# Kernel tuning notes

Hardware: AMD Instinct MI355X
Metric: run time of the kernel (lower is better)

Reference implementation:

```python
import jax, jax.numpy as jnp
import numpy as np

TTT_LR = 0.01
LN_EPS = 1e-5


def setup_inputs() -> dict:
    key = jax.random.key(0)
    ks = jax.random.split(key, 4)
    B, S, D, DS = 4, 2048, 1024, 64
    sc = 1.0 / np.sqrt(D).astype(np.float32)
    return {
        "x": jax.random.normal(ks[0], (B, S, D), dtype=jnp.float32),
        "Wk": jax.random.normal(ks[1], (DS, D), dtype=jnp.float32) * sc,
        "bk": jnp.zeros((DS,), jnp.float32),
        "Wv": jax.random.normal(ks[2], (D, D), dtype=jnp.float32) * sc,
        "bv": jnp.zeros((D,), jnp.float32),
        "Wq": jax.random.normal(ks[3], (DS, D), dtype=jnp.float32) * sc,
        "bq": jnp.zeros((DS,), jnp.float32),
        "gamma": jnp.ones((D,), jnp.float32),
        "beta": jnp.zeros((D,), jnp.float32),
    }


def reference(x, Wk, bk, Wv, bv, Wq, bq, gamma, beta):
    B, S, D = x.shape
    DS = Wk.shape[0]
    # LayerNorm over last dim
    mu = jnp.mean(x, axis=-1, keepdims=True)
    var = jnp.mean((x - mu) ** 2, axis=-1, keepdims=True)
    h = (x - mu) * jax.lax.rsqrt(var + LN_EPS) * gamma + beta
    # projections: keys/queries (B,S,DS), values (B,S,D)
    keys = jnp.einsum('bsd,ed->bse', h, Wk) + bk
    values = jnp.einsum('bsd,ed->bse', h, Wv) + bv
    queries = jnp.einsum('bsd,ed->bse', h, Wq) + bq

    def step(W, qkv):
        # W: (B, D, DS) fast-weight state
        q_t, k_t, v_t = qkv  # (B,DS), (B,DS), (B,D)
        y_t = jnp.einsum('bds,bs->bd', W, q_t)      # read with query
        pred = jnp.einsum('bds,bs->bd', W, k_t)     # predict with key
        err = pred - v_t                             # (B, D)
        W = W - TTT_LR * err[:, :, None] * k_t[:, None, :]  # rank-1 grad step
        return W, y_t

    W0 = jnp.zeros((B, D, DS), x.dtype)
    # scan over time: inputs as (S, B, ...)
    qs = jnp.swapaxes(queries, 0, 1)
    ks_ = jnp.swapaxes(keys, 0, 1)
    vs = jnp.swapaxes(values, 0, 1)
    _, ys = jax.lax.scan(step, W0, (qs, ks_, vs))   # ys: (S, B, D)
    y = jnp.swapaxes(ys, 0, 1)
    return x + y
```

## Files before the change

### kernel.cpp

```cpp
#include <hip/hip_runtime.h>
#include <hip/hip_bf16.h>

#define TTT_LR 0.01f
#define LN_EPS 1e-5f

#define BB 4
#define SS 2048
#define DD 1024
#define DSZ 64
#define CHUNK 64
#define NC (SS / CHUNK)
#define NCAT 1152
#define NCVT (NCAT * DD / 4 / 256)
#define MiB (1024ull * 1024ull)

typedef __hip_bfloat16 bf16;
typedef __bf16 bf16x8 __attribute__((ext_vector_type(8)));
typedef float f32x4 __attribute__((ext_vector_type(4)));

__device__ __forceinline__ void gload_lds16(const void* g, void* l) {
    __builtin_amdgcn_global_load_lds(
        (const __attribute__((address_space(1))) unsigned int*)g,
        (__attribute__((address_space(3))) unsigned int*)l, 16, 0, 0);
}

__global__ __launch_bounds__(256) void pre_kernel(
    const float* __restrict__ Wk, const float* __restrict__ Wq,
    const float* __restrict__ Wv, bf16* __restrict__ Wcat,
    const float* __restrict__ x, const float* __restrict__ gamma,
    const float* __restrict__ beta, bf16* __restrict__ hb)
{
    __shared__ float wsum[4], wsum2[4];
    const int tid = threadIdx.x;

    if (blockIdx.x < NCVT) {
        const int i = blockIdx.x * 256 + tid;
        const int idx = i * 4;
        const int row = idx >> 10, col = idx & 1023;
        const float* src = (row < 64)  ? (Wk + (size_t)row * DD)
                         : (row < 128) ? (Wq + (size_t)(row - 64) * DD)
                                       : (Wv + (size_t)(row - 128) * DD);
        float4 v = *reinterpret_cast<const float4*>(src + col);
        bf16 h4[4] = {__float2bfloat16(v.x), __float2bfloat16(v.y),
                      __float2bfloat16(v.z), __float2bfloat16(v.w)};
        *reinterpret_cast<ushort4*>(Wcat + idx) = *reinterpret_cast<ushort4*>(h4);
        return;
    }

    const int row = blockIdx.x - NCVT;
    const int lane = tid & 63, wave = tid >> 6;

    float4 v0 = *reinterpret_cast<const float4*>(x + (size_t)row * DD + tid * 4);
    float s = v0.x + v0.y + v0.z + v0.w;
    float s2 = fmaf(v0.x, v0.x, fmaf(v0.y, v0.y, fmaf(v0.z, v0.z, v0.w * v0.w)));
    #pragma unroll
    for (int off = 32; off > 0; off >>= 1) {
        s  += __shfl_down(s, off, 64);
        s2 += __shfl_down(s2, off, 64);
    }
    if (lane == 0) { wsum[wave] = s; wsum2[wave] = s2; }
    __syncthreads();
    s  = wsum[0] + wsum[1] + wsum[2] + wsum[3];
    s2 = wsum2[0] + wsum2[1] + wsum2[2] + wsum2[3];
    const float mu = s * (1.0f / DD);
    const float rs = rsqrtf(s2 * (1.0f / DD) - mu * mu + LN_EPS);

    float4 g  = *reinterpret_cast<const float4*>(gamma + tid * 4);
    float4 be = *reinterpret_cast<const float4*>(beta + tid * 4);
    bf16 h4[4];
    h4[0] = __float2bfloat16((v0.x - mu) * rs * g.x + be.x);
    h4[1] = __float2bfloat16((v0.y - mu) * rs * g.y + be.y);
    h4[2] = __float2bfloat16((v0.z - mu) * rs * g.z + be.z);
    h4[3] = __float2bfloat16((v0.w - mu) * rs * g.w + be.w);
    *reinterpret_cast<ushort4*>(hb + (size_t)row * DD + tid * 4) =
        *reinterpret_cast<ushort4*>(h4);
}

__global__ __launch_bounds__(256) void kqv_kernel(
    const bf16* __restrict__ h, const bf16* __restrict__ Wcat,
    const float* __restrict__ bk, const float* __restrict__ bq,
    const float* __restrict__ bv,
    float* __restrict__ kbuf, float* __restrict__ qbuf, bf16* __restrict__ vbuf16)
{
    __shared__ bf16 Ash[128 * 64];
    __shared__ bf16 Bsh[128 * 64];
    const int tid = threadIdx.x, lane = tid & 63, wave = tid >> 6;
    const int m = lane & 15, quad = lane >> 4;
    const int wr = wave >> 1, wc = wave & 1;
    const int m0 = blockIdx.y * 128;
    const int n0 = blockIdx.x * 128;

    const int srow = wave * 8 + (lane >> 3);
    const int scb = lane & 7;

    f32x4 acc[4][4] = {};

    for (int k0 = 0; k0 < DD; k0 += 64) {
        __syncthreads();
        #pragma unroll
        for (int i = 0; i < 4; ++i) {
            const int row = i * 32 + srow;
            const int g16 = scb ^ (row & 7);
            gload_lds16(h    + (size_t)(m0 + row) * DD + k0 + g16 * 8,
                        (char*)Ash + (size_t)(i * 32 + wave * 8) * 128);
            gload_lds16(Wcat + (size_t)(n0 + row) * DD + k0 + g16 * 8,
                        (char*)Bsh + (size_t)(i * 32 + wave * 8) * 128);
        }
        __syncthreads();
        #pragma unroll
        for (int ks = 0; ks < 2; ++ks) {
            bf16x8 af[4], bfr[4];
            #pragma unroll
            for (int mt = 0; mt < 4; ++mt) {
                const int row = wr * 64 + mt * 16 + m;
                const int kb = (ks * 4 + quad) ^ (row & 7);
                af[mt] = *reinterpret_cast<const bf16x8*>(&Ash[row * 64 + kb * 8]);
            }
            #pragma unroll
            for (int nt = 0; nt < 4; ++nt) {
                const int row = wc * 64 + nt * 16 + m;
                const int kb = (ks * 4 + quad) ^ (row & 7);
                bfr[nt] = *reinterpret_cast<const bf16x8*>(&Bsh[row * 64 + kb * 8]);
            }
            #pragma unroll
            for (int mt = 0; mt < 4; ++mt)
                #pragma unroll
                for (int nt = 0; nt < 4; ++nt)
                    acc[mt][nt] = __builtin_amdgcn_mfma_f32_16x16x32_bf16(
                        af[mt], bfr[nt], acc[mt][nt], 0, 0, 0);
        }
    }

    #pragma unroll
    for (int nt = 0; nt < 4; ++nt) {
        const int n = n0 + wc * 64 + nt * 16 + m;
        if (n < 64) {
            const float bias = bk[n];
            #pragma unroll
            for (int mt = 0; mt < 4; ++mt) {
                const int row = m0 + wr * 64 + mt * 16 + quad * 4;
                #pragma unroll
                for (int r = 0; r < 4; ++r)
                    kbuf[(size_t)(row + r) * DSZ + n] = acc[mt][nt][r] + bias;
            }
        } else if (n < 128) {
            const float bias = bq[n - 64];
            #pragma unroll
            for (int mt = 0; mt < 4; ++mt) {
                const int row = m0 + wr * 64 + mt * 16 + quad * 4;
                #pragma unroll
                for (int r = 0; r < 4; ++r)
                    qbuf[(size_t)(row + r) * DSZ + (n - 64)] = acc[mt][nt][r] + bias;
            }
        } else {
            const float bias = bv[n - 128];
            #pragma unroll
            for (int mt = 0; mt < 4; ++mt) {
                const int row = m0 + wr * 64 + mt * 16 + quad * 4;
                #pragma unroll
                for (int r = 0; r < 4; ++r)
                    vbuf16[(size_t)(row + r) * DD + (n - 128)] =
                        __float2bfloat16(acc[mt][nt][r] + bias);
            }
        }
    }
}

__global__ __launch_bounds__(256) void prep_kernel(
    const float* __restrict__ kbuf, const float* __restrict__ qbuf,
    bf16* __restrict__ Mb16, bf16* __restrict__ AMb16,
    bf16* __restrict__ Bb16, bf16* __restrict__ Qtb16, bf16* __restrict__ Ktb16)
{
    __shared__ bf16 K16[64 * 72];
    __shared__ bf16 Kt16[64 * 72];
    __shared__ bf16 Q16[64 * 72];
    __shared__ bf16 Astl[64 * 72];
    __shared__ bf16 Minv16[64 * 72];
    __shared__ bf16 MinvT16[64 * 72];
    __shared__ bf16 BnegT[64 * 72];
    __shared__ float Gf[64 * 65];
    __shared__ float Mf[64 * 65];

    const int c = blockIdx.x, b = blockIdx.y;
    const int tid = threadIdx.x, lane = tid & 63, w = tid >> 6;
    const int m = lane & 15, quad = lane >> 4;
    const float* kp = kbuf + ((size_t)b * SS + c * 64) * DSZ;
    const float* qp = qbuf + ((size_t)b * SS + c * 64) * DSZ;
    const size_t cb = ((size_t)b * NC + c) * 4096;

    #pragma unroll
    for (int it = 0; it < 4; ++it) {
        const int f4 = tid + it * 256;
        const int t = f4 >> 4;
        const int s = (f4 & 15) * 4;
        float4 kv = *reinterpret_cast<const float4*>(kp + t * DSZ + s);
        float4 qv = *reinterpret_cast<const float4*>(qp + t * DSZ + s);
        bf16 kb4[4] = {__float2bfloat16(kv.x), __float2bfloat16(kv.y),
                       __float2bfloat16(kv.z), __float2bfloat16(kv.w)};
        bf16 qb4[4] = {__float2bfloat16(qv.x), __float2bfloat16(qv.y),
                       __float2bfloat16(qv.z), __float2bfloat16(qv.w)};
        *reinterpret_cast<ushort4*>(&K16[t * 72 + s]) = *reinterpret_cast<ushort4*>(kb4);
        *reinterpret_cast<ushort4*>(&Q16[t * 72 + s]) = *reinterpret_cast<ushort4*>(qb4);
        #pragma unroll
        for (int i = 0; i < 4; ++i) Kt16[(s + i) * 72 + t] = kb4[i];
    }
    __syncthreads();

    bf16x8 afK[2], afQ[2], bfK[4][2];
    #pragma unroll
    for (int ks = 0; ks < 2; ++ks) {
        afK[ks] = *reinterpret_cast<const bf16x8*>(&K16[(w * 16 + m) * 72 + ks * 32 + quad * 8]);
        afQ[ks] = *reinterpret_cast<const bf16x8*>(&Q16[(w * 16 + m) * 72 + ks * 32 + quad * 8]);
        #pragma unroll
        for (int nt = 0; nt < 4; ++nt)
            bfK[nt][ks] = *reinterpret_cast<const bf16x8*>(&K16[(nt * 16 + m) * 72 + ks * 32 + quad * 8]);
    }
    f32x4 gacc[4] = {}, aacc[4] = {};
    #pragma unroll
    for (int ks = 0; ks < 2; ++ks)
        #pragma unroll
        for (int nt = 0; nt < 4; ++nt) {
            gacc[nt] = __builtin_amdgcn_mfma_f32_16x16x32_bf16(afK[ks], bfK[nt][ks], gacc[nt], 0, 0, 0);
            aacc[nt] = __builtin_amdgcn_mfma_f32_16x16x32_bf16(afQ[ks], bfK[nt][ks], aacc[nt], 0, 0, 0);
        }
    #pragma unroll
    for (int nt = 0; nt < 4; ++nt)
        #pragma unroll
        for (int r = 0; r < 4; ++r) {
            const int t = w * 16 + quad * 4 + r, j = nt * 16 + m;
            Gf[t * 65 + j] = TTT_LR * gacc[nt][r];
            Astl[t * 72 + j] = __float2bfloat16(j < t ? aacc[nt][r] : 0.f);
        }
    __syncthreads();

    if (tid < 64) {
        for (int t = 0; t < 64; ++t) {
            float acc = (t == tid) ? 1.f : 0.f;
            for (int i = 0; i < t; ++i)
                acc = fmaf(-Gf[t * 65 + i], Mf[i * 65 + tid], acc);
            Mf[t * 65 + tid] = acc;
        }
    }
    __syncthreads();

    #pragma unroll
    for (int it = 0; it < 16; ++it) {
        const int e = tid + it * 256;
        const int t = e >> 6, j = e & 63;
        const bf16 vb = __float2bfloat16(TTT_LR * Mf[t * 65 + j]);
        Minv16[t * 72 + j] = vb;
        MinvT16[j * 72 + t] = vb;
        Mb16[cb + e] = vb;
        const unsigned short ku =
            *reinterpret_cast<const unsigned short*>(&Kt16[t * 72 + j]) ^ 0x8000u;
        *reinterpret_cast<unsigned short*>(&Ktb16[cb + e]) = ku;
    }
    __syncthreads();

    bf16x8 afM[2], afA[2], bfKt[4][2], bfMt[4][2];
    #pragma unroll
    for (int ks = 0; ks < 2; ++ks) {
        afM[ks] = *reinterpret_cast<const bf16x8*>(&Minv16[(w * 16 + m) * 72 + ks * 32 + quad * 8]);
        afA[ks] = *reinterpret_cast<const bf16x8*>(&Astl[(w * 16 + m) * 72 + ks * 32 + quad * 8]);
        #pragma unroll
        for (int nt = 0; nt < 4; ++nt) {
            bfKt[nt][ks] = *reinterpret_cast<const bf16x8*>(&Kt16[(nt * 16 + m) * 72 + ks * 32 + quad * 8]);
            bfMt[nt][ks] = *reinterpret_cast<const bf16x8*>(&MinvT16[(nt * 16 + m) * 72 + ks * 32 + quad * 8]);
        }
    }
    f32x4 bacc[4] = {};
    #pragma unroll
    for (int ks = 0; ks < 2; ++ks)
        #pragma unroll
        for (int nt = 0; nt < 4; ++nt)
            bacc[nt] = __builtin_amdgcn_mfma_f32_16x16x32_bf16(afM[ks], bfKt[nt][ks], bacc[nt], 0, 0, 0);
    #pragma unroll
    for (int nt = 0; nt < 4; ++nt)
        #pragma unroll
        for (int r = 0; r < 4; ++r) {
            const int t = w * 16 + quad * 4 + r, s = nt * 16 + m;
            Bb16[cb + t * 64 + s] = __float2bfloat16(bacc[nt][r]);
            BnegT[s * 72 + t] = __float2bfloat16(-bacc[nt][r]);
        }
    __syncthreads();

    f32x4 qtacc[4], amacc[4] = {};
    #pragma unroll
    for (int nt = 0; nt < 4; ++nt)
        #pragma unroll
        for (int r = 0; r < 4; ++r)
            qtacc[nt][r] = qp[(w * 16 + quad * 4 + r) * DSZ + nt * 16 + m];
    #pragma unroll
    for (int ks = 0; ks < 2; ++ks)
        #pragma unroll
        for (int nt = 0; nt < 4; ++nt) {
            const bf16x8 bfBn = *reinterpret_cast<const bf16x8*>(
                &BnegT[(nt * 16 + m) * 72 + ks * 32 + quad * 8]);
            qtacc[nt] = __builtin_amdgcn_mfma_f32_16x16x32_bf16(afA[ks], bfBn, qtacc[nt], 0, 0, 0);
            amacc[nt] = __builtin_amdgcn_mfma_f32_16x16x32_bf16(afA[ks], bfMt[nt][ks], amacc[nt], 0, 0, 0);
        }
    #pragma unroll
    for (int nt = 0; nt < 4; ++nt)
        #pragma unroll
        for (int r = 0; r < 4; ++r) {
            const int t = w * 16 + quad * 4 + r, s = nt * 16 + m;
            Qtb16[cb + t * 64 + s] = __float2bfloat16(qtacc[nt][r]);
            AMb16[cb + t * 64 + s] = __float2bfloat16(amacc[nt][r]);
        }
}

struct ChunkRegs {
    bf16x8 M0, M1, A0, A1, B0, B1, Q0, Q1, K0, K1;
    alignas(8) unsigned short va[4], vb[4];
    float xld[4];
};

__global__ __launch_bounds__(256) void scan2_kernel(
    const bf16* __restrict__ Mb16, const bf16* __restrict__ AMb16,
    const bf16* __restrict__ Bb16, const bf16* __restrict__ Qtb16,
    const bf16* __restrict__ Ktb16, const bf16* __restrict__ v16,
    const float* __restrict__ x, float* __restrict__ out)
{
    __shared__ bf16 Zsh[16][72];
    __shared__ bf16 Psh[16][72];
    __shared__ bf16 Vsh[2][16][72];
    const int dblk = blockIdx.x, b = blockIdx.y;
    const int tid = threadIdx.x, lane = tid & 63, w = tid >> 6;
    const int m = lane & 15, quad = lane >> 4;
    const int d0 = dblk * 16;
    const int arow = w * 16 + m;
    const int trow = w * 16 + quad * 4;

    const bool vact = tid < 128;
    const int vj2 = (tid & 31) * 2;
    const int vd = (tid >> 5) * 4;

    f32x4 zacc = {0.f, 0.f, 0.f, 0.f};
    for (int i = tid; i < 16 * 72; i += 256)
        (&Zsh[0][0])[i] = __float2bfloat16(0.f);

    auto load_chunk = [&](int c, ChunkRegs& R) {
        const size_t cb = ((size_t)b * NC + c) * 4096;
        const size_t rowbase = (size_t)b * SS + (size_t)c * 64;
        R.M0 = *reinterpret_cast<const bf16x8*>(Mb16 + cb + arow * 64 + quad * 8);
        R.M1 = *reinterpret_cast<const bf16x8*>(Mb16 + cb + arow * 64 + 32 + quad * 8);
        R.A0 = *reinterpret_cast<const bf16x8*>(AMb16 + cb + arow * 64 + quad * 8);
        R.A1 = *reinterpret_cast<const bf16x8*>(AMb16 + cb + arow * 64 + 32 + quad * 8);
        R.B0 = *reinterpret_cast<const bf16x8*>(Bb16 + cb + arow * 64 + quad * 8);
        R.B1 = *reinterpret_cast<const bf16x8*>(Bb16 + cb + arow * 64 + 32 + quad * 8);
        R.Q0 = *reinterpret_cast<const bf16x8*>(Qtb16 + cb + arow * 64 + quad * 8);
        R.Q1 = *reinterpret_cast<const bf16x8*>(Qtb16 + cb + arow * 64 + 32 + quad * 8);
        R.K0 = *reinterpret_cast<const bf16x8*>(Ktb16 + cb + arow * 64 + quad * 8);
        R.K1 = *reinterpret_cast<const bf16x8*>(Ktb16 + cb + arow * 64 + 32 + quad * 8);
        if (vact) {
            *reinterpret_cast<uint2*>(R.va) = *reinterpret_cast<const uint2*>(
                v16 + (rowbase + vj2) * DD + d0 + vd);
            *reinterpret_cast<uint2*>(R.vb) = *reinterpret_cast<const uint2*>(
                v16 + (rowbase + vj2 + 1) * DD + d0 + vd);
        }
        const size_t gbase = (rowbase + trow) * DD + d0 + m;
        #pragma unroll
        for (int r = 0; r < 4; ++r) R.xld[r] = x[gbase + (size_t)r * DD];
    };

    auto stage_v = [&](const ChunkRegs& R, int buf) {
        if (vact) {
            #pragma unroll
            for (int i = 0; i < 4; ++i) {
                const unsigned int pack =
                    (unsigned int)R.va[i] | ((unsigned int)R.vb[i] << 16);
                *reinterpret_cast<unsigned int*>(&Vsh[buf][vd + i][vj2]) = pack;
            }
        }
    };

    auto compute = [&](const ChunkRegs& R, int c, int buf) {
        const size_t gbase = ((size_t)b * SS + (size_t)c * 64 + trow) * DD + d0 + m;
        const bf16x8 z0 = *reinterpret_cast<const bf16x8*>(&Zsh[m][quad * 8]);
        const bf16x8 z1 = *reinterpret_cast<const bf16x8*>(&Zsh[m][32 + quad * 8]);
        const bf16x8 v0 = *reinterpret_cast<const bf16x8*>(&Vsh[buf][m][quad * 8]);
        const bf16x8 v1 = *reinterpret_cast<const bf16x8*>(&Vsh[buf][m][32 + quad * 8]);

        f32x4 uacc = {0.f, 0.f, 0.f, 0.f};
        f32x4 yi   = {0.f, 0.f, 0.f, 0.f};
        f32x4 pacc = {0.f, 0.f, 0.f, 0.f};
        f32x4 yc   = {0.f, 0.f, 0.f, 0.f};
        uacc = __builtin_amdgcn_mfma_f32_16x16x32_bf16(R.M0, v0, uacc, 0, 0, 0);
        uacc = __builtin_amdgcn_mfma_f32_16x16x32_bf16(R.M1, v1, uacc, 0, 0, 0);
        yi   = __builtin_amdgcn_mfma_f32_16x16x32_bf16(R.A0, v0, yi, 0, 0, 0);
        yi   = __builtin_amdgcn_mfma_f32_16x16x32_bf16(R.A1, v1, yi, 0, 0, 0);
        pacc = __builtin_amdgcn_mfma_f32_16x16x32_bf16(R.B0, z0, pacc, 0, 0, 0);
        pacc = __builtin_amdgcn_mfma_f32_16x16x32_bf16(R.B1, z1, pacc, 0, 0, 0);
        yc   = __builtin_amdgcn_mfma_f32_16x16x32_bf16(R.Q0, z0, yc, 0, 0, 0);
        yc   = __builtin_amdgcn_mfma_f32_16x16x32_bf16(R.Q1, z1, yc, 0, 0, 0);

        alignas(8) bf16 pb[4];
        #pragma unroll
        for (int r = 0; r < 4; ++r) {
            out[gbase + (size_t)r * DD] = R.xld[r] + yi[r] + yc[r];
            pb[r] = __float2bfloat16(pacc[r] - uacc[r]);
        }
        *reinterpret_cast<uint2*>(&Psh[m][trow]) = *reinterpret_cast<uint2*>(pb);

        __syncthreads();
        const bf16x8 p0 = *reinterpret_cast<const bf16x8*>(&Psh[m][quad * 8]);
        const bf16x8 p1 = *reinterpret_cast<const bf16x8*>(&Psh[m][32 + quad * 8]);
        zacc = __builtin_amdgcn_mfma_f32_16x16x32_bf16(R.K0, p0, zacc, 0, 0, 0);
        zacc = __builtin_amdgcn_mfma_f32_16x16x32_bf16(R.K1, p1, zacc, 0, 0, 0);

        alignas(8) bf16 zb[4];
        #pragma unroll
        for (int r = 0; r < 4; ++r) zb[r] = __float2bfloat16(zacc[r]);
        *reinterpret_cast<uint2*>(&Zsh[m][trow]) = *reinterpret_cast<uint2*>(zb);
    };

    ChunkRegs R0, R1;
    load_chunk(0, R0);
    for (int c = 0; c < NC; c += 2) {
        stage_v(R0, 0);
        __syncthreads();
        load_chunk(c + 1, R1);
        compute(R0, c, 0);
        stage_v(R1, 1);
        __syncthreads();
        if (c + 2 < NC) load_chunk(c + 2, R0);
        compute(R1, c + 1, 1);
    }
}

extern "C" void kernel_launch(void* const* d_in, const int* in_sizes, int n_in,
                              void* d_out, int out_size, void* d_ws, size_t ws_size,
                              hipStream_t stream)
{
    const float* x     = (const float*)d_in[0];
    const float* Wk    = (const float*)d_in[1];
    const float* bk    = (const float*)d_in[2];
    const float* Wv    = (const float*)d_in[3];
    const float* bv    = (const float*)d_in[4];
    const float* Wq    = (const float*)d_in[5];
    const float* bq    = (const float*)d_in[6];
    const float* gamma = (const float*)d_in[7];
    const float* beta  = (const float*)d_in[8];

    char* ws = (char*)d_ws;
    const size_t WCAT_B = (size_t)NCAT * DD * 2;
    bf16*  hb    = (bf16*)ws;
    bf16*  Bb16  = (bf16*)(ws + 0 * MiB);
    bf16*  Qtb16 = (bf16*)(ws + 1 * MiB);
    bf16*  Ktb16 = (bf16*)(ws + 2 * MiB);
    bf16*  Mb16  = (bf16*)(ws + 3 * MiB);
    bf16*  AMb16 = (bf16*)(ws + 4 * MiB);
    bf16*  Wcat  = (bf16*)(ws + 16 * MiB);
    float* kbuf  = (float*)(ws + 16 * MiB + WCAT_B);
    float* qbuf  = (float*)(ws + 18 * MiB + WCAT_B);
    bf16*  v16   = (bf16*)(ws + 20 * MiB + WCAT_B);

    pre_kernel<<<NCVT + BB * SS, 256, 0, stream>>>(
        Wk, Wq, Wv, Wcat, x, gamma, beta, hb);
    kqv_kernel<<<dim3(NCAT / 128, BB * SS / 128), 256, 0, stream>>>(
        hb, Wcat, bk, bq, bv, kbuf, qbuf, v16);
    prep_kernel<<<dim3(NC, BB), 256, 0, stream>>>(
        kbuf, qbuf, Mb16, AMb16, Bb16, Qtb16, Ktb16);
    scan2_kernel<<<dim3(DD / 16, BB), 256, 0, stream>>>(
        Mb16, AMb16, Bb16, Qtb16, Ktb16, v16, x, (float*)d_out);
}
```

Before: 229.3 us.

## Fold per-chunk state update into precomputed transition matrices, removing mid-chunk barrier

New measurement: 221.6 us. 1.03x faster.

```diff
diff --git a/kernel.cpp b/kernel.cpp
--- a/kernel.cpp
+++ b/kernel.cpp
@@ -168,8 +168,8 @@
 
 __global__ __launch_bounds__(256) void prep_kernel(
     const float* __restrict__ kbuf, const float* __restrict__ qbuf,
-    bf16* __restrict__ Mb16, bf16* __restrict__ AMb16,
-    bf16* __restrict__ Bb16, bf16* __restrict__ Qtb16, bf16* __restrict__ Ktb16)
+    bf16* __restrict__ Tb16, bf16* __restrict__ Wb16,
+    bf16* __restrict__ AMb16, bf16* __restrict__ Qtb16)
 {
     __shared__ bf16 K16[64 * 72];
     __shared__ bf16 Kt16[64 * 72];
@@ -250,18 +250,15 @@
         const bf16 vb = __float2bfloat16(TTT_LR * Mf[t * 65 + j]);
         Minv16[t * 72 + j] = vb;
         MinvT16[j * 72 + t] = vb;
-        Mb16[cb + e] = vb;
-        const unsigned short ku =
-            *reinterpret_cast<const unsigned short*>(&Kt16[t * 72 + j]) ^ 0x8000u;
-        *reinterpret_cast<unsigned short*>(&Ktb16[cb + e]) = ku;
-    }
-    __syncthreads();
-
-    bf16x8 afM[2], afA[2], bfKt[4][2], bfMt[4][2];
+    }
+    __syncthreads();
+
+    bf16x8 afM[2], afA[2], afKt[2], bfKt[4][2], bfMt[4][2];
     #pragma unroll
     for (int ks = 0; ks < 2; ++ks) {
-        afM[ks] = *reinterpret_cast<const bf16x8*>(&Minv16[(w * 16 + m) * 72 + ks * 32 + quad * 8]);
-        afA[ks] = *reinterpret_cast<const bf16x8*>(&Astl[(w * 16 + m) * 72 + ks * 32 + quad * 8]);
+        afM[ks]  = *reinterpret_cast<const bf16x8*>(&Minv16[(w * 16 + m) * 72 + ks * 32 + quad * 8]);
+        afA[ks]  = *reinterpret_cast<const bf16x8*>(&Astl[(w * 16 + m) * 72 + ks * 32 + quad * 8]);
+        afKt[ks] = *reinterpret_cast<const bf16x8*>(&Kt16[(w * 16 + m) * 72 + ks * 32 + quad * 8]);
         #pragma unroll
         for (int nt = 0; nt < 4; ++nt) {
             bfKt[nt][ks] = *reinterpret_cast<const bf16x8*>(&Kt16[(nt * 16 + m) * 72 + ks * 32 + quad * 8]);
@@ -279,12 +276,11 @@
         #pragma unroll
         for (int r = 0; r < 4; ++r) {
             const int t = w * 16 + quad * 4 + r, s = nt * 16 + m;
-            Bb16[cb + t * 64 + s] = __float2bfloat16(bacc[nt][r]);
             BnegT[s * 72 + t] = __float2bfloat16(-bacc[nt][r]);
         }
     __syncthreads();
 
-    f32x4 qtacc[4], amacc[4] = {};
+    f32x4 qtacc[4], amacc[4] = {}, tacc[4] = {}, wacc[4] = {};
     #pragma unroll
     for (int nt = 0; nt < 4; ++nt)
         #pragma unroll
@@ -298,31 +294,34 @@
                 &BnegT[(nt * 16 + m) * 72 + ks * 32 + quad * 8]);
             qtacc[nt] = __builtin_amdgcn_mfma_f32_16x16x32_bf16(afA[ks], bfBn, qtacc[nt], 0, 0, 0);
             amacc[nt] = __builtin_amdgcn_mfma_f32_16x16x32_bf16(afA[ks], bfMt[nt][ks], amacc[nt], 0, 0, 0);
+            tacc[nt]  = __builtin_amdgcn_mfma_f32_16x16x32_bf16(afKt[ks], bfBn, tacc[nt], 0, 0, 0);
+            wacc[nt]  = __builtin_amdgcn_mfma_f32_16x16x32_bf16(afKt[ks], bfMt[nt][ks], wacc[nt], 0, 0, 0);
         }
     #pragma unroll
     for (int nt = 0; nt < 4; ++nt)
         #pragma unroll
         for (int r = 0; r < 4; ++r) {
-            const int t = w * 16 + quad * 4 + r, s = nt * 16 + m;
-            Qtb16[cb + t * 64 + s] = __float2bfloat16(qtacc[nt][r]);
-            AMb16[cb + t * 64 + s] = __float2bfloat16(amacc[nt][r]);
+            const int row = w * 16 + quad * 4 + r, col = nt * 16 + m;
+            Qtb16[cb + row * 64 + col] = __float2bfloat16(qtacc[nt][r]);
+            AMb16[cb + row * 64 + col] = __float2bfloat16(amacc[nt][r]);
+            Tb16[cb + row * 64 + col]  = __float2bfloat16(tacc[nt][r]);
+            Wb16[cb + row * 64 + col]  = __float2bfloat16(wacc[nt][r]);
         }
 }
 
 struct ChunkRegs {
-    bf16x8 M0, M1, A0, A1, B0, B1, Q0, Q1, K0, K1;
+    bf16x8 T0, T1, W0, W1, A0, A1, Q0, Q1;
     alignas(8) unsigned short va[4], vb[4];
     float xld[4];
 };
 
 __global__ __launch_bounds__(256) void scan2_kernel(
-    const bf16* __restrict__ Mb16, const bf16* __restrict__ AMb16,
-    const bf16* __restrict__ Bb16, const bf16* __restrict__ Qtb16,
-    const bf16* __restrict__ Ktb16, const bf16* __restrict__ v16,
-    const float* __restrict__ x, float* __restrict__ out)
+    const bf16* __restrict__ Tb16, const bf16* __restrict__ Wb16,
+    const bf16* __restrict__ AMb16, const bf16* __restrict__ Qtb16,
+    const bf16* __restrict__ v16, const float* __restrict__ x,
+    float* __restrict__ out)
 {
-    __shared__ bf16 Zsh[16][72];
-    __shared__ bf16 Psh[16][72];
+    __shared__ bf16 Zsh[2][16][72];
     __shared__ bf16 Vsh[2][16][72];
     const int dblk = blockIdx.x, b = blockIdx.y;
     const int tid = threadIdx.x, lane = tid & 63, w = tid >> 6;
@@ -337,21 +336,19 @@
 
     f32x4 zacc = {0.f, 0.f, 0.f, 0.f};
     for (int i = tid; i < 16 * 72; i += 256)
-        (&Zsh[0][0])[i] = __float2bfloat16(0.f);
+        (&Zsh[0][0][0])[i] = __float2bfloat16(0.f);
 
     auto load_chunk = [&](int c, ChunkRegs& R) {
         const size_t cb = ((size_t)b * NC + c) * 4096;
         const size_t rowbase = (size_t)b * SS + (size_t)c * 64;
-        R.M0 = *reinterpret_cast<const bf16x8*>(Mb16 + cb + arow * 64 + quad * 8);
-        R.M1 = *reinterpret_cast<const bf16x8*>(Mb16 + cb + arow * 64 + 32 + quad * 8);
+        R.T0 = *reinterpret_cast<const bf16x8*>(Tb16 + cb + arow * 64 + quad * 8);
+        R.T1 = *reinterpret_cast<const bf16x8*>(Tb16 + cb + arow * 64 + 32 + quad * 8);
+        R.W0 = *reinterpret_cast<const bf16x8*>(Wb16 + cb + arow * 64 + quad * 8);
+        R.W1 = *reinterpret_cast<const bf16x8*>(Wb16 + cb + arow * 64 + 32 + quad * 8);
         R.A0 = *reinterpret_cast<const bf16x8*>(AMb16 + cb + arow * 64 + quad * 8);
         R.A1 = *reinterpret_cast<const bf16x8*>(AMb16 + cb + arow * 64 + 32 + quad * 8);
-        R.B0 = *reinterpret_cast<const bf16x8*>(Bb16 + cb + arow * 64 + quad * 8);
-        R.B1 = *reinterpret_cast<const bf16x8*>(Bb16 + cb + arow * 64 + 32 + quad * 8);
         R.Q0 = *reinterpret_cast<const bf16x8*>(Qtb16 + cb + arow * 64 + quad * 8);
         R.Q1 = *reinterpret_cast<const bf16x8*>(Qtb16 + cb + arow * 64 + 32 + quad * 8);
-        R.K0 = *reinterpret_cast<const bf16x8*>(Ktb16 + cb + arow * 64 + quad * 8);
-        R.K1 = *reinterpret_cast<const bf16x8*>(Ktb16 + cb + arow * 64 + 32 + quad * 8);
         if (vact) {
             *reinterpret_cast<uint2*>(R.va) = *reinterpret_cast<const uint2*>(
                 v16 + (rowbase + vj2) * DD + d0 + vd);
@@ -376,42 +373,31 @@
 
     auto compute = [&](const ChunkRegs& R, int c, int buf) {
         const size_t gbase = ((size_t)b * SS + (size_t)c * 64 + trow) * DD + d0 + m;
-        const bf16x8 z0 = *reinterpret_cast<const bf16x8*>(&Zsh[m][quad * 8]);
-        const bf16x8 z1 = *reinterpret_cast<const bf16x8*>(&Zsh[m][32 + quad * 8]);
+        const bf16x8 z0 = *reinterpret_cast<const bf16x8*>(&Zsh[buf][m][quad * 8]);
+        const bf16x8 z1 = *reinterpret_cast<const bf16x8*>(&Zsh[buf][m][32 + quad * 8]);
         const bf16x8 v0 = *reinterpret_cast<const bf16x8*>(&Vsh[buf][m][quad * 8]);
         const bf16x8 v1 = *reinterpret_cast<const bf16x8*>(&Vsh[buf][m][32 + quad * 8]);
 
-        f32x4 uacc = {0.f, 0.f, 0.f, 0.f};
-        f32x4 yi   = {0.f, 0.f, 0.f, 0.f};
-        f32x4 pacc = {0.f, 0.f, 0.f, 0.f};
-        f32x4 yc   = {0.f, 0.f, 0.f, 0.f};
-        uacc = __builtin_amdgcn_mfma_f32_16x16x32_bf16(R.M0, v0, uacc, 0, 0, 0);
-        uacc = __builtin_amdgcn_mfma_f32_16x16x32_bf16(R.M1, v1, uacc, 0, 0, 0);
-        yi   = __builtin_amdgcn_mfma_f32_16x16x32_bf16(R.A0, v0, yi, 0, 0, 0);
-        yi   = __builtin_amdgcn_mfma_f32_16x16x32_bf16(R.A1, v1, yi, 0, 0, 0);
-        pacc = __builtin_amdgcn_mfma_f32_16x16x32_bf16(R.B0, z0, pacc, 0, 0, 0);
-        pacc = __builtin_amdgcn_mfma_f32_16x16x32_bf16(R.B1, z1, pacc, 0, 0, 0);
-        yc   = __builtin_amdgcn_mfma_f32_16x16x32_bf16(R.Q0, z0, yc, 0, 0, 0);
-        yc   = __builtin_amdgcn_mfma_f32_16x16x32_bf16(R.Q1, z1, yc, 0, 0, 0);
-
-        alignas(8) bf16 pb[4];
-        #pragma unroll
-        for (int r = 0; r < 4; ++r) {
-            out[gbase + (size_t)r * DD] = R.xld[r] + yi[r] + yc[r];
-            pb[r] = __float2bfloat16(pacc[r] - uacc[r]);
-        }
-        *reinterpret_cast<uint2*>(&Psh[m][trow]) = *reinterpret_cast<uint2*>(pb);
-
-        __syncthreads();
-        const bf16x8 p0 = *reinterpret_cast<const bf16x8*>(&Psh[m][quad * 8]);
-        const bf16x8 p1 = *reinterpret_cast<const bf16x8*>(&Psh[m][32 + quad * 8]);
-        zacc = __builtin_amdgcn_mfma_f32_16x16x32_bf16(R.K0, p0, zacc, 0, 0, 0);
-        zacc = __builtin_amdgcn_mfma_f32_16x16x32_bf16(R.K1, p1, zacc, 0, 0, 0);
+        zacc = __builtin_amdgcn_mfma_f32_16x16x32_bf16(R.T0, z0, zacc, 0, 0, 0);
+        zacc = __builtin_amdgcn_mfma_f32_16x16x32_bf16(R.T1, z1, zacc, 0, 0, 0);
+        zacc = __builtin_amdgcn_mfma_f32_16x16x32_bf16(R.W0, v0, zacc, 0, 0, 0);
+        zacc = __builtin_amdgcn_mfma_f32_16x16x32_bf16(R.W1, v1, zacc, 0, 0, 0);
+
+        f32x4 y = {0.f, 0.f, 0.f, 0.f};
+        y = __builtin_amdgcn_mfma_f32_16x16x32_bf16(R.Q0, z0, y, 0, 0, 0);
+        y = __builtin_amdgcn_mfma_f32_16x16x32_bf16(R.Q1, z1, y, 0, 0, 0);
+        y = __builtin_amdgcn_mfma_f32_16x16x32_bf16(R.A0, v0, y, 0, 0, 0);
+        y = __builtin_amdgcn_mfma_f32_16x16x32_bf16(R.A1, v1, y, 0, 0, 0);
 
         alignas(8) bf16 zb[4];
         #pragma unroll
         for (int r = 0; r < 4; ++r) zb[r] = __float2bfloat16(zacc[r]);
-        *reinterpret_cast<uint2*>(&Zsh[m][trow]) = *reinterpret_cast<uint2*>(zb);
+        *reinterpret_cast<uint2*>(&Zsh[buf ^ 1][m][trow]) =
+            *reinterpret_cast<uint2*>(zb);
+
+        #pragma unroll
+        for (int r = 0; r < 4; ++r)
+            out[gbase + (size_t)r * DD] = R.xld[r] + y[r];
     };
 
     ChunkRegs R0, R1;
@@ -445,11 +431,10 @@
     char* ws = (char*)d_ws;
     const size_t WCAT_B = (size_t)NCAT * DD * 2;
     bf16*  hb    = (bf16*)ws;
-    bf16*  Bb16  = (bf16*)(ws + 0 * MiB);
+    bf16*  Tb16  = (bf16*)(ws + 0 * MiB);
     bf16*  Qtb16 = (bf16*)(ws + 1 * MiB);
-    bf16*  Ktb16 = (bf16*)(ws + 2 * MiB);
-    bf16*  Mb16  = (bf16*)(ws + 3 * MiB);
-    bf16*  AMb16 = (bf16*)(ws + 4 * MiB);
+    bf16*  Wb16  = (bf16*)(ws + 2 * MiB);
+    bf16*  AMb16 = (bf16*)(ws + 3 * MiB);
     bf16*  Wcat  = (bf16*)(ws + 16 * MiB);
     float* kbuf  = (float*)(ws + 16 * MiB + WCAT_B);
     float* qbuf  = (float*)(ws + 18 * MiB + WCAT_B);
@@ -460,7 +445,7 @@
     kqv_kernel<<<dim3(NCAT / 128, BB * SS / 128), 256, 0, stream>>>(
         hb, Wcat, bk, bq, bv, kbuf, qbuf, v16);
     prep_kernel<<<dim3(NC, BB), 256, 0, stream>>>(
-        kbuf, qbuf, Mb16, AMb16, Bb16, Qtb16, Ktb16);
+        kbuf, qbuf, Tb16, Wb16, AMb16, Qtb16);
     scan2_kernel<<<dim3(DD / 16, BB), 256, 0, stream>>>(
-        Mb16, AMb16, Bb16, Qtb16, Ktb16, v16, x, (float*)d_out);
-}
+        Tb16, Wb16, AMb16, Qtb16, v16, x, (float*)d_out);
+}
```
